# Kernel optimization log

Measured on AMD Instinct MI355X. Metric: run time of the kernel, lower is better.

## Reference

```python
import jax, jax.numpy as jnp
import numpy as np

B, S, DIM = 2, 2048, 2048
H, KVH, HD = 16, 4, 128
G = H // KVH  # GQA groups = 4
THETA = 10000.0


def setup_inputs() -> dict:
    key = jax.random.key(0)
    k0, k1, k2, k3, k4 = jax.random.split(key, 5)
    x = jax.random.normal(k0, (B, S, DIM), jnp.float32)
    # RoPE table: [max_seq_len, head_dim//2, 2] holding (cos, sin)
    inv_freq = 1.0 / (THETA ** (jnp.arange(0, HD, 2, dtype=jnp.float32) / HD))
    angles = jnp.outer(jnp.arange(S, dtype=jnp.float32), inv_freq)  # [S, HD//2]
    freqs_cis = jnp.stack([jnp.cos(angles), jnp.sin(angles)], axis=-1)
    sc = 0.02
    wq = jax.random.normal(k1, (H * HD, DIM), jnp.float32) * sc
    wk = jax.random.normal(k2, (KVH * HD, DIM), jnp.float32) * sc
    wv = jax.random.normal(k3, (KVH * HD, DIM), jnp.float32) * sc
    wo = jax.random.normal(k4, (DIM, H * HD), jnp.float32) * sc
    return {"x": x, "freqs_cis": freqs_cis, "wq": wq, "wk": wk, "wv": wv, "wo": wo}


def apply_rope(x, freqs_cis):
    # x: [B, S, h, HD]; freqs_cis: [max_S, HD//2, 2]
    s = x.shape[1]
    xr = x.astype(jnp.float32).reshape(*x.shape[:-1], -1, 2)  # [B,S,h,HD//2,2]
    cos = freqs_cis[:s, :, 0][None, :, None, :]  # [1,S,1,HD//2]
    sin = freqs_cis[:s, :, 1][None, :, None, :]
    x0, x1 = xr[..., 0], xr[..., 1]
    out = jnp.stack([x0 * cos - x1 * sin, x0 * sin + x1 * cos], axis=-1)
    return out.reshape(x.shape).astype(x.dtype)


def reference(x, freqs_cis, wq, wk, wv, wo):
    b, s, d = x.shape
    q = (x @ wq.T).reshape(b, s, H, HD)
    k = (x @ wk.T).reshape(b, s, KVH, HD)
    v = (x @ wv.T).reshape(b, s, KVH, HD)
    q = apply_rope(q, freqs_cis)
    k = apply_rope(k, freqs_cis)
    # GQA expand: repeat_interleave along head dim
    k = jnp.repeat(k, G, axis=2)  # [b,s,H,HD]
    v = jnp.repeat(v, G, axis=2)
    q = jnp.swapaxes(q, 1, 2)  # [b,H,s,HD]
    k = jnp.swapaxes(k, 1, 2)
    v = jnp.swapaxes(v, 1, 2)
    scale = 1.0 / jnp.sqrt(jnp.asarray(HD, dtype=q.dtype))
    scores = jnp.einsum('bhqd,bhkd->bhqk', q, k) * scale  # [b,H,s,s]
    causal = jnp.tril(jnp.ones((s, s), dtype=bool))
    scores = jnp.where(causal[None, None], scores, jnp.finfo(scores.dtype).min)
    probs = jax.nn.softmax(scores, axis=-1)
    attn = jnp.einsum('bhqk,bhkd->bhqd', probs, v)  # [b,H,s,HD]
    attn = jnp.swapaxes(attn, 1, 2).reshape(b, s, H * HD)
    return attn @ wo.T
```

## Files before the change

### kernel.cpp

```cpp
#include <hip/hip_runtime.h>
#include <stdint.h>

#define B_ 2
#define S_ 2048
#define DIM_ 2048
#define H_ 16
#define KVH_ 4
#define HD_ 128

typedef short short8 __attribute__((ext_vector_type(8)));
typedef float f4 __attribute__((ext_vector_type(4)));
typedef float f16v __attribute__((ext_vector_type(16)));
typedef unsigned int uint2v __attribute__((ext_vector_type(2)));
typedef unsigned short u16;

#define KSCALE (0.08838834764831845f * 1.4426950408889634f)

__device__ __forceinline__ float bf2f(u16 u) {
    union { unsigned int i; float f; } c; c.i = ((unsigned int)u) << 16; return c.f;
}
__device__ __forceinline__ u16 f2bf(float f) {
    union { float f; unsigned int i; } c; c.f = f;
    return (u16)((c.i + 0x7fffu + ((c.i >> 16) & 1u)) >> 16);
}
__device__ __forceinline__ unsigned pk_bf16(float lo, float hi) {
    unsigned r;
    asm("v_cvt_pk_bf16_f32 %0, %1, %2" : "=v"(r) : "v"(lo), "v"(hi));
    return r;
}

#define GLDS16(gp, lp) \
    __builtin_amdgcn_global_load_lds((const __attribute__((address_space(1))) unsigned int*)(gp), \
                                     (__attribute__((address_space(3))) unsigned int*)(lp), 16, 0, 0)

#define BAR()     asm volatile("s_barrier" ::: "memory")
#define WAITLGKM() asm volatile("s_waitcnt lgkmcnt(0)" ::: "memory")
#define SCHEDB()  __builtin_amdgcn_sched_barrier(0)

__global__ void cast_all(const float* __restrict__ x,  const float* __restrict__ wq,
                         const float* __restrict__ wk, const float* __restrict__ wv,
                         const float* __restrict__ wo,
                         u16* __restrict__ xb, u16* __restrict__ wqkvb, u16* __restrict__ wob) {
    int i = blockIdx.x * 256 + threadIdx.x;
    const float4* src; ushort4* dst; int j;
    if (i < 2097152)      { src = (const float4*)x;  dst = (ushort4*)xb;                 j = i; }
    else if (i < 3145728) { src = (const float4*)wq; dst = (ushort4*)wqkvb;              j = i - 2097152; }
    else if (i < 3407872) { src = (const float4*)wk; dst = (ushort4*)wqkvb + 1048576;    j = i - 3145728; }
    else if (i < 3670016) { src = (const float4*)wv; dst = (ushort4*)wqkvb + 1310720;    j = i - 3407872; }
    else                  { src = (const float4*)wo; dst = (ushort4*)wob;                j = i - 3670016; }
    float4 v = src[j];
    ushort4 o;
    o.x = f2bf(v.x); o.y = f2bf(v.y); o.z = f2bf(v.z); o.w = f2bf(v.w);
    dst[j] = o;
}

template<bool OUT_BF16, int NBX>
__global__ __launch_bounds__(512, 2) void gemm256(const u16* __restrict__ A,
                                                  const u16* __restrict__ W,
                                                  void* __restrict__ Cout,
                                                  int M, int N, int K) {
    __shared__ u16 As[2][16384];
    __shared__ u16 Bs[2][16384];
    int t = threadIdx.x, lane = t & 63, w = t >> 6;
    int quad = lane >> 4, l16 = lane & 15, l7 = lane & 7;
    int wm = w >> 2, wn = w & 3;
    int bid = blockIdx.x;
    int xcd = bid & 7, grp = bid >> 3;
    int bx = grp % NBX, by = (grp / NBX) * 8 + xcd;
    size_t m0 = (size_t)by * 256, n0 = (size_t)bx * 256;

    int srow = lane >> 3;
    int sunit = (lane & 7) ^ srow;
    int rR0a = (w >> 2) * 64 + (w & 3) * 8;
    const u16* Ag = A + (m0 + srow) * (size_t)K + sunit * 8;
    const u16* Bg = W + (n0 + srow) * (size_t)K + sunit * 8;

#define STG_A(pl, tk, r0) GLDS16(Ag + ((size_t)((r0) + w * 8)) * K + (tk) * 64, (pl) + ((r0) + w * 8) * 64)
#define STG_B(pl, tk, r0) GLDS16(Bg + ((size_t)((r0) + w * 8)) * K + (tk) * 64, (pl) + ((r0) + w * 8) * 64)
#define STG_BR(pl, tk, bse) GLDS16(Bg + ((size_t)((bse) + rR0a)) * K + (tk) * 64, (pl) + ((bse) + rR0a) * 64)

#define LDA(mh) { \
    _Pragma("unroll") for (int i_ = 0; i_ < 4; i_++) \
    _Pragma("unroll") for (int k_ = 0; k_ < 2; k_++) \
        a[i_][k_] = *(const short8*)&pAc[(wm * 128 + (mh) * 64 + i_ * 16 + l16) * 64 + (((quad + 4 * k_) ^ l7) << 3)]; }
#define LDB(nh) { \
    _Pragma("unroll") for (int j_ = 0; j_ < 2; j_++) \
    _Pragma("unroll") for (int k_ = 0; k_ < 2; k_++) \
        b[j_][k_] = *(const short8*)&pBc[(wn * 64 + (nh) * 32 + j_ * 16 + l16) * 64 + (((quad + 4 * k_) ^ l7) << 3)]; }
#define MFMA_Q(mh, nh) { \
    __builtin_amdgcn_s_setprio(1); \
    _Pragma("unroll") for (int i_ = 0; i_ < 4; i_++) \
    _Pragma("unroll") for (int j_ = 0; j_ < 2; j_++) \
    _Pragma("unroll") for (int k_ = 0; k_ < 2; k_++) \
        acc[(mh) * 4 + i_][(nh) * 2 + j_] = __builtin_amdgcn_mfma_f32_16x16x32_bf16( \
            a[i_][k_], b[j_][k_], acc[(mh) * 4 + i_][(nh) * 2 + j_], 0, 0, 0); \
    __builtin_amdgcn_s_setprio(0); }

    f4 acc[8][4];
    #pragma unroll
    for (int i = 0; i < 8; i++)
        #pragma unroll
        for (int j = 0; j < 4; j++) acc[i][j] = (f4){0.f, 0.f, 0.f, 0.f};

    int NT = K >> 6;

    #pragma unroll
    for (int pt = 0; pt < 2; pt++) {
        u16* pa = &As[pt][0]; u16* pb = &Bs[pt][0];
        #pragma unroll
        for (int r0 = 0; r0 < 256; r0 += 64) { STG_A(pa, pt, r0); STG_B(pb, pt, r0); }
    }
    asm volatile("s_waitcnt vmcnt(0)" ::: "memory");
    BAR();

    short8 a[4][2], b[2][2];
    for (int tt = 0; tt < NT; tt++) {
        int c = tt & 1, nc = c ^ 1;
        u16* pAc = &As[c][0];  u16* pBc = &Bs[c][0];
        u16* pAn = &As[nc][0]; u16* pBn = &Bs[nc][0];
        bool s1 = (tt >= 1) & (tt + 1 < NT);
        bool s2 = (tt + 2 < NT);
        LDA(0); LDB(0);
        if (s1) { STG_A(pAn, tt + 1, 64); STG_A(pAn, tt + 1, 192); }
        BAR(); WAITLGKM(); MFMA_Q(0, 0); BAR();
        LDB(1);
        if (s1) { STG_BR(pBn, tt + 1, 32); STG_BR(pBn, tt + 1, 160); }
        BAR(); WAITLGKM(); MFMA_Q(0, 1); BAR();
        LDA(1); LDB(0);
        if (s2) { STG_A(pAc, tt + 2, 0); STG_A(pAc, tt + 2, 128); }
        BAR(); WAITLGKM(); MFMA_Q(1, 0); BAR();
        if (s2) asm volatile("s_waitcnt vmcnt(2)" ::: "memory");
        else    asm volatile("s_waitcnt vmcnt(0)" ::: "memory");
        LDB(1);
        if (s2) { STG_BR(pBc, tt + 2, 0); STG_BR(pBc, tt + 2, 128); }
        BAR(); WAITLGKM(); MFMA_Q(1, 1); BAR();
    }

    #pragma unroll
    for (int i = 0; i < 8; i++) {
        size_t row = m0 + wm * 128 + i * 16 + quad * 4;
        #pragma unroll
        for (int j = 0; j < 4; j++) {
            size_t col = n0 + wn * 64 + j * 16 + l16;
            #pragma unroll
            for (int r = 0; r < 4; r++) {
                if (OUT_BF16) ((u16*)Cout)[(row + r) * (size_t)N + col] = f2bf(acc[i][j][r]);
                else          ((float*)Cout)[(row + r) * (size_t)N + col] = acc[i][j][r];
            }
        }
    }
#undef STG_A
#undef STG_B
#undef STG_BR
#undef LDA
#undef LDB
#undef MFMA_Q
}

__global__ __launch_bounds__(256) void pack_k(const u16* __restrict__ QKV,
                                              const float* __restrict__ freqs,
                                              u16* __restrict__ Kp) {
    int gid = blockIdx.x * 256 + threadIdx.x;
    int lane = gid & 63, j = (gid >> 6) & 1, ds = (gid >> 7) & 7;
    int kt = (gid >> 10) & 31, bk = gid >> 15;
    int b = bk >> 2, kvh = bk & 3;
    int l31 = lane & 31, hi = lane >> 5;
    int s = kt * 64 + j * 32 + l31;
    int d0 = ds * 16 + hi * 8;
    const u16* src = QKV + (size_t)(b * S_ + s) * 3072 + 2048 + kvh * HD_ + d0;
    short8 v = *(const short8*)src;
    short8 o;
    #pragma unroll
    for (int jp = 0; jp < 4; jp++) {
        float2 cw = ((const float2*)freqs)[s * 64 + ds * 8 + hi * 4 + jp];
        float x0 = bf2f((u16)v[2 * jp]), x1 = bf2f((u16)v[2 * jp + 1]);
        o[2 * jp]     = (short)f2bf(x0 * cw.x - x1 * cw.y);
        o[2 * jp + 1] = (short)f2bf(x0 * cw.y + x1 * cw.x);
    }
    *(short8*)&Kp[(size_t)gid * 8] = o;
}

__global__ __launch_bounds__(256) void pack_v(const u16* __restrict__ QKV, u16* __restrict__ Vp) {
    __shared__ u16 L[64 * 136];
    int bid = blockIdx.x;
    int bk = bid & 7, kt = bid >> 3;
    int b = bk >> 2, kvh = bk & 3;
    int t = threadIdx.x;
    const u16* src = QKV + (size_t)(b * S_ + kt * 64) * 3072 + 2560 + kvh * HD_;
    #pragma unroll
    for (int it = 0; it < 4; it++) {
        int idx = t + it * 256;
        int r = idx >> 4, c = idx & 15;
        *(short8*)&L[r * 136 + c * 8] = *(const short8*)(src + (size_t)r * 3072 + c * 8);
    }
    __syncthreads();
    u16* dst = Vp + (size_t)(bk * 32 + kt) * 8192;
    #pragma unroll
    for (int it = 0; it < 4; it++) {
        int idx = t + it * 256;
        int frag = idx >> 6, lane = idx & 63;
        int ks = frag >> 2, ht = frag & 3;
        int hd = ht * 32 + (lane & 31);
        int k0 = ks * 16 + (lane >> 5) * 8;
        short8 v;
        #pragma unroll
        for (int jj = 0; jj < 8; jj++) v[jj] = (short)L[(k0 + jj) * 136 + hd];
        *(short8*)&dst[(size_t)idx * 8] = v;
    }
}

__global__ __launch_bounds__(64, 1)
void attn_kernel(const u16* __restrict__ QKV,
                 const float* __restrict__ freqs,
                 const u16* __restrict__ Kp,
                 const u16* __restrict__ Vp,
                 u16* __restrict__ Ob) {
    int bid = blockIdx.x;
    int k8 = bid >> 8;
    int c  = bid & 255;
    int bk = c & 7, h4 = (c >> 3) & 3, tq = c >> 5;
    int qb = 63 - (k8 * 8 + ((k8 & 1) ? 7 - tq : tq));
    int b = bk >> 2, kvh = bk & 3;
    int lane = threadIdx.x;
    int l31 = lane & 31, hi = lane >> 5;
    int h = kvh * 4 + h4;
    int nkt = (qb >> 1) + 1;

    short8 qf[8];
    {
        int s = qb * 32 + l31;
        const u16* qp = QKV + ((size_t)(b * S_ + s)) * 3072 + h * HD_ + hi * 8;
        const float2* fr2 = (const float2*)freqs;
        #pragma unroll
        for (int ds = 0; ds < 8; ds++) {
            short8 v = *(const short8*)(qp + ds * 16);
            short8 o;
            #pragma unroll
            for (int jp = 0; jp < 4; jp++) {
                float2 cs = fr2[s * 64 + ds * 8 + hi * 4 + jp];
                float x0 = bf2f((u16)v[2 * jp]), x1 = bf2f((u16)v[2 * jp + 1]);
                o[2 * jp]     = (short)f2bf((x0 * cs.x - x1 * cs.y) * KSCALE);
                o[2 * jp + 1] = (short)f2bf((x0 * cs.y + x1 * cs.x) * KSCALE);
            }
            qf[ds] = o;
        }
    }

    float m_i = -3e38f, ls = 0.f;
    f16v o4[4];
    #pragma unroll
    for (int i = 0; i < 4; i++)
        #pragma unroll
        for (int r = 0; r < 16; r++) o4[i][r] = 0.f;

    const u16* Kpb = Kp + (size_t)bk * 32 * 8192 + lane * 8;
    const u16* Vpb = Vp + (size_t)bk * 32 * 8192 + lane * 8;

    short8 kf[16];
    #pragma unroll
    for (int f = 0; f < 16; f++) kf[f] = *(const short8*)(Kpb + f * 512);

    for (int kt = 0; kt < nkt; kt++) {
        short8 vf[16];
        {
            const u16* vb = Vpb + (size_t)kt * 8192;
            #pragma unroll
            for (int f = 0; f < 16; f++) vf[f] = *(const short8*)(vb + f * 512);
        }
        SCHEDB();

        f16v sA[2], sB[2];
        #pragma unroll
        for (int k2 = 0; k2 < 2; k2++)
            #pragma unroll
            for (int r = 0; r < 16; r++) { sA[k2][r] = 0.f; sB[k2][r] = 0.f; }
        __builtin_amdgcn_s_setprio(1);
        #pragma unroll
        for (int ds = 0; ds < 4; ds++) {
            sA[0] = __builtin_amdgcn_mfma_f32_32x32x16_bf16(kf[ds * 2],     qf[ds], sA[0], 0, 0, 0);
            sA[1] = __builtin_amdgcn_mfma_f32_32x32x16_bf16(kf[ds * 2 + 1], qf[ds], sA[1], 0, 0, 0);
            sB[0] = __builtin_amdgcn_mfma_f32_32x32x16_bf16(kf[(ds + 4) * 2],     qf[ds + 4], sB[0], 0, 0, 0);
            sB[1] = __builtin_amdgcn_mfma_f32_32x32x16_bf16(kf[(ds + 4) * 2 + 1], qf[ds + 4], sB[1], 0, 0, 0);
        }
        __builtin_amdgcn_s_setprio(0);
        SCHEDB();

        if (kt + 1 < nkt) {
            const u16* kb = Kpb + (size_t)(kt + 1) * 8192;
            #pragma unroll
            for (int f = 0; f < 16; f++) kf[f] = *(const short8*)(kb + f * 512);
        }
        SCHEDB();

        f16v sacc[2];
        #pragma unroll
        for (int k2 = 0; k2 < 2; k2++)
            #pragma unroll
            for (int r = 0; r < 16; r++) sacc[k2][r] = sA[k2][r] + sB[k2][r];

        if (kt == nkt - 1) {
            int off0 = kt * 64 - qb * 32;
            #pragma unroll
            for (int k2 = 0; k2 < 2; k2++) {
                #pragma unroll
                for (int r = 0; r < 16; r++) {
                    int colo = off0 + k2 * 32 + (r & 3) + ((r >> 2) << 3) + (hi << 2);
                    if (colo > l31) sacc[k2][r] = -3e38f;
                }
            }
        }

        float mx[16];
        #pragma unroll
        for (int r = 0; r < 16; r++) mx[r] = fmaxf(sacc[0][r], sacc[1][r]);
        #pragma unroll
        for (int s_ = 8; s_ > 0; s_ >>= 1)
            #pragma unroll
            for (int r = 0; r < s_; r++) mx[r] = fmaxf(mx[r], mx[r + s_]);
        float pm = fmaxf(mx[0], __shfl_xor(mx[0], 32, 64));
        if (__any(pm > m_i + 8.0f)) {
            float mnew = fmaxf(m_i, pm);
            float al = exp2f(m_i - mnew);
            ls *= al;
            #pragma unroll
            for (int i = 0; i < 4; i++)
                #pragma unroll
                for (int r = 0; r < 16; r++) o4[i][r] *= al;
            m_i = mnew;
        }

        short8 pa[4];
        #pragma unroll
        for (int k2 = 0; k2 < 2; k2++) {
            float p[16];
            #pragma unroll
            for (int r = 0; r < 16; r++) p[r] = exp2f(sacc[k2][r] - m_i);
            float s0 = (p[0] + p[1]) + (p[2] + p[3]);
            float s1 = (p[4] + p[5]) + (p[6] + p[7]);
            float s2 = (p[8] + p[9]) + (p[10] + p[11]);
            float s3 = (p[12] + p[13]) + (p[14] + p[15]);
            ls += (s0 + s1) + (s2 + s3);
            unsigned W0 = pk_bf16(p[0], p[1]),   W1 = pk_bf16(p[2], p[3]);
            unsigned W2 = pk_bf16(p[4], p[5]),   W3 = pk_bf16(p[6], p[7]);
            unsigned W4 = pk_bf16(p[8], p[9]),   W5 = pk_bf16(p[10], p[11]);
            unsigned W6 = pk_bf16(p[12], p[13]), W7 = pk_bf16(p[14], p[15]);
            uint2v r02 = __builtin_amdgcn_permlane32_swap(W0, W2, false, false);
            uint2v r13 = __builtin_amdgcn_permlane32_swap(W1, W3, false, false);
            uint2v r46 = __builtin_amdgcn_permlane32_swap(W4, W6, false, false);
            uint2v r57 = __builtin_amdgcn_permlane32_swap(W5, W7, false, false);
            union { unsigned u[4]; short8 s8; } flo, fhi;
            flo.u[0] = r02[0]; flo.u[1] = r13[0]; flo.u[2] = r02[1]; flo.u[3] = r13[1];
            fhi.u[0] = r46[0]; fhi.u[1] = r57[0]; fhi.u[2] = r46[1]; fhi.u[3] = r57[1];
            pa[k2 * 2]     = flo.s8;
            pa[k2 * 2 + 1] = fhi.s8;
        }
        SCHEDB();

        __builtin_amdgcn_s_setprio(1);
        #pragma unroll
        for (int ks = 0; ks < 4; ks++) {
            #pragma unroll
            for (int ht = 0; ht < 4; ht++)
                o4[ht] = __builtin_amdgcn_mfma_f32_32x32x16_bf16(vf[ks * 4 + ht], pa[ks], o4[ht], 0, 0, 0);
        }
        __builtin_amdgcn_s_setprio(0);
    }

    ls += __shfl_xor(ls, 32, 64);
    float rl = 1.0f / ls;
    size_t row = (size_t)b * S_ + qb * 32 + l31;
    u16* op = Ob + row * 2048 + h * HD_;
    #pragma unroll
    for (int ht = 0; ht < 4; ht++) {
        #pragma unroll
        for (int g = 0; g < 4; g++) {
            ushort4 st;
            st.x = f2bf(o4[ht][4 * g + 0] * rl);
            st.y = f2bf(o4[ht][4 * g + 1] * rl);
            st.z = f2bf(o4[ht][4 * g + 2] * rl);
            st.w = f2bf(o4[ht][4 * g + 3] * rl);
            *(ushort4*)&op[ht * 32 + g * 8 + hi * 4] = st;
        }
    }
}

extern "C" void kernel_launch(void* const* d_in, const int* in_sizes, int n_in,
                              void* d_out, int out_size, void* d_ws, size_t ws_size,
                              hipStream_t stream) {
    const float* x     = (const float*)d_in[0];
    const float* freqs = (const float*)d_in[1];
    const float* wq    = (const float*)d_in[2];
    const float* wk    = (const float*)d_in[3];
    const float* wv    = (const float*)d_in[4];
    const float* wo    = (const float*)d_in[5];
    float* out = (float*)d_out;

    char* p = (char*)d_ws;
    u16* xb    = (u16*)p; p += (size_t)4096 * 2048 * 2;
    u16* wqkvb = (u16*)p; p += (size_t)3072 * 2048 * 2;
    u16* wob   = (u16*)p; p += (size_t)2048 * 2048 * 2;
    u16* QKVb  = (u16*)p; p += (size_t)4096 * 3072 * 2;
    u16* Kpb   = (u16*)p; p += (size_t)8 * 32 * 8192 * 2;
    u16* Vpb   = (u16*)p; p += (size_t)8 * 32 * 8192 * 2;
    u16* attnb = xb;

    cast_all<<<18432, 256, 0, stream>>>(x, wq, wk, wv, wo, xb, wqkvb, wob);

    gemm256<true, 12><<<192, 512, 0, stream>>>(xb, wqkvb, QKVb, 4096, 3072, 2048);

    pack_k<<<1024, 256, 0, stream>>>(QKVb, freqs, Kpb);
    pack_v<<<256, 256, 0, stream>>>(QKVb, Vpb);

    attn_kernel<<<2048, 64, 0, stream>>>(QKVb, freqs, Kpb, Vpb, attnb);

    gemm256<false, 8><<<128, 512, 0, stream>>>(attnb, wob, out, 4096, 2048, 2048);
}
```

Measured before the change: 318.0 us.

## Split long causal query blocks across two KV chunks with a combine kernel

Query blocks in the upper half of the sequence (qb 32..63) now have their KV loop split into two workgroups, one covering KV tiles 0-15 and one covering the rest. Each writes unnormalized fp32 partial outputs plus its running max and sum to workspace, and a new combine kernel rescales and merges the pairs. The aim is to balance work across the grid and shorten the critical-path workgroups of the causal attention. The cost is an extra kernel launch, partial-output writes and reads, and a path that only runs when the workspace is large enough.

Result: slower. 352.1 us (+10.7%).

```diff
diff --git a/kernel.cpp b/kernel.cpp
--- a/kernel.cpp
+++ b/kernel.cpp
@@ -214,12 +214,34 @@
                  const float* __restrict__ freqs,
                  const u16* __restrict__ Kp,
                  const u16* __restrict__ Vp,
-                 u16* __restrict__ Ob) {
+                 u16* __restrict__ Ob,
+                 float* __restrict__ Po,
+                 float* __restrict__ Pm,
+                 int split) {
     int bid = blockIdx.x;
-    int k8 = bid >> 8;
-    int c  = bid & 255;
-    int bk = c & 7, h4 = (c >> 3) & 3, tq = c >> 5;
-    int qb = 63 - (k8 * 8 + ((k8 & 1) ? 7 - tq : tq));
+    int bk, h4, qb, kt0, kt1, slot = -1;
+    if (split) {
+        int c = bid & 255, t = bid >> 8;
+        bk = c & 7; h4 = (c >> 3) & 3;
+        int tau = t * 8 + (c >> 5);
+        if (tau < 64) {
+            qb = 32 + (tau >> 1);
+            int nkt_ = (qb >> 1) + 1;
+            int ck = tau & 1;
+            kt0 = ck ? 16 : 0;
+            kt1 = ck ? nkt_ : 16;
+            slot = ((bk * 4 + h4) * 32 + (qb - 32)) * 2 + ck;
+        } else {
+            qb = tau - 64;
+            kt0 = 0; kt1 = (qb >> 1) + 1;
+        }
+    } else {
+        int k8 = bid >> 8, c = bid & 255;
+        bk = c & 7; h4 = (c >> 3) & 3;
+        int tq = c >> 5;
+        qb = 63 - (k8 * 8 + ((k8 & 1) ? 7 - tq : tq));
+        kt0 = 0; kt1 = (qb >> 1) + 1;
+    }
     int b = bk >> 2, kvh = bk & 3;
     int lane = threadIdx.x;
     int l31 = lane & 31, hi = lane >> 5;
@@ -257,10 +279,13 @@
     const u16* Vpb = Vp + (size_t)bk * 32 * 8192 + lane * 8;
 
     short8 kf[16];
-    #pragma unroll
-    for (int f = 0; f < 16; f++) kf[f] = *(const short8*)(Kpb + f * 512);
-
-    for (int kt = 0; kt < nkt; kt++) {
+    {
+        const u16* kb = Kpb + (size_t)kt0 * 8192;
+        #pragma unroll
+        for (int f = 0; f < 16; f++) kf[f] = *(const short8*)(kb + f * 512);
+    }
+
+    for (int kt = kt0; kt < kt1; kt++) {
         short8 vf[16];
         {
             const u16* vb = Vpb + (size_t)kt * 8192;
@@ -285,7 +310,7 @@
         __builtin_amdgcn_s_setprio(0);
         SCHEDB();
 
-        if (kt + 1 < nkt) {
+        if (kt + 1 < kt1) {
             const u16* kb = Kpb + (size_t)(kt + 1) * 8192;
             #pragma unroll
             for (int f = 0; f < 16; f++) kf[f] = *(const short8*)(kb + f * 512);
@@ -367,18 +392,63 @@
     }
 
     ls += __shfl_xor(ls, 32, 64);
-    float rl = 1.0f / ls;
+    if (slot >= 0) {
+        float* po = Po + (size_t)slot * 4096 + lane * 64;
+        #pragma unroll
+        for (int ht = 0; ht < 4; ht++)
+            #pragma unroll
+            for (int r = 0; r < 16; r++) po[ht * 16 + r] = o4[ht][r];
+        Pm[(size_t)slot * 128 + lane * 2]     = m_i;
+        Pm[(size_t)slot * 128 + lane * 2 + 1] = ls;
+    } else {
+        float rl = 1.0f / ls;
+        size_t row = (size_t)b * S_ + qb * 32 + l31;
+        u16* op = Ob + row * 2048 + h * HD_;
+        #pragma unroll
+        for (int ht = 0; ht < 4; ht++) {
+            #pragma unroll
+            for (int g = 0; g < 4; g++) {
+                ushort4 st;
+                st.x = f2bf(o4[ht][4 * g + 0] * rl);
+                st.y = f2bf(o4[ht][4 * g + 1] * rl);
+                st.z = f2bf(o4[ht][4 * g + 2] * rl);
+                st.w = f2bf(o4[ht][4 * g + 3] * rl);
+                *(ushort4*)&op[ht * 32 + g * 8 + hi * 4] = st;
+            }
+        }
+    }
+}
+
+__global__ __launch_bounds__(64) void attn_combine(const float* __restrict__ Po,
+                                                   const float* __restrict__ Pm,
+                                                   u16* __restrict__ Ob) {
+    int cid = blockIdx.x;
+    int bk = cid & 7, h4 = (cid >> 3) & 3, qq = cid >> 5;
+    int qb = 32 + qq;
+    int b = bk >> 2, kvh = bk & 3;
+    int h = kvh * 4 + h4;
+    int lane = threadIdx.x;
+    int l31 = lane & 31, hi = lane >> 5;
+    int s0 = ((bk * 4 + h4) * 32 + qq) * 2;
+    float m0 = Pm[(size_t)s0 * 128 + lane * 2],       l0 = Pm[(size_t)s0 * 128 + lane * 2 + 1];
+    float m1 = Pm[(size_t)(s0 + 1) * 128 + lane * 2], l1 = Pm[(size_t)(s0 + 1) * 128 + lane * 2 + 1];
+    float M  = fmaxf(m0, m1);
+    float a0 = exp2f(m0 - M), a1 = exp2f(m1 - M);
+    float rl = 1.0f / (l0 * a0 + l1 * a1);
+    const float4* q0 = (const float4*)(Po + (size_t)s0 * 4096 + lane * 64);
+    const float4* q1 = (const float4*)(Po + (size_t)(s0 + 1) * 4096 + lane * 64);
     size_t row = (size_t)b * S_ + qb * 32 + l31;
     u16* op = Ob + row * 2048 + h * HD_;
     #pragma unroll
     for (int ht = 0; ht < 4; ht++) {
         #pragma unroll
         for (int g = 0; g < 4; g++) {
+            float4 v0 = q0[ht * 4 + g], v1 = q1[ht * 4 + g];
             ushort4 st;
-            st.x = f2bf(o4[ht][4 * g + 0] * rl);
-            st.y = f2bf(o4[ht][4 * g + 1] * rl);
-            st.z = f2bf(o4[ht][4 * g + 2] * rl);
-            st.w = f2bf(o4[ht][4 * g + 3] * rl);
+            st.x = f2bf((v0.x * a0 + v1.x * a1) * rl);
+            st.y = f2bf((v0.y * a0 + v1.y * a1) * rl);
+            st.z = f2bf((v0.z * a0 + v1.z * a1) * rl);
+            st.w = f2bf((v0.w * a0 + v1.w * a1) * rl);
             *(ushort4*)&op[ht * 32 + g * 8 + hi * 4] = st;
         }
     }
@@ -402,7 +472,12 @@
     u16* QKVb  = (u16*)p; p += (size_t)4096 * 3072 * 2;
     u16* Kpb   = (u16*)p; p += (size_t)8 * 32 * 8192 * 2;
     u16* Vpb   = (u16*)p; p += (size_t)8 * 32 * 8192 * 2;
+    float* Po  = (float*)p; p += (size_t)2048 * 4096 * 4;
+    float* Pm  = (float*)p; p += (size_t)2048 * 128 * 4;
     u16* attnb = xb;
+
+    size_t need = (size_t)(p - (char*)d_ws);
+    int split = (ws_size >= need) ? 1 : 0;
 
     cast_all<<<18432, 256, 0, stream>>>(x, wq, wk, wv, wo, xb, wqkvb, wob);
 
@@ -411,7 +486,12 @@
     pack_k<<<1024, 256, 0, stream>>>(QKVb, freqs, Kpb);
     pack_v<<<256, 256, 0, stream>>>(QKVb, Vpb);
 
-    attn_kernel<<<2048, 64, 0, stream>>>(QKVb, freqs, Kpb, Vpb, attnb);
+    if (split) {
+        attn_kernel<<<3072, 64, 0, stream>>>(QKVb, freqs, Kpb, Vpb, attnb, Po, Pm, 1);
+        attn_combine<<<1024, 64, 0, stream>>>(Po, Pm, attnb);
+    } else {
+        attn_kernel<<<2048, 64, 0, stream>>>(QKVb, freqs, Kpb, Vpb, attnb, Po, Pm, 0);
+    }
 
     gemm256<false, 8><<<128, 512, 0, stream>>>(attnb, wob, out, 4096, 2048, 2048);
 }
```

## Process two adjacent query blocks per wave to reuse K/V fragments

Applied to the files above, without the earlier changes.

Each single-wave block now handles an even and an odd 32-row query block that share the same 64-key tiles. Every loaded K and V fragment therefore feeds twice as many MFMAs, and half as many blocks are launched. The work order is remapped into four balanced ranges to even out the causal load. The cost is a doubled accumulator and Q register footprint, which raises register pressure and may cause spills. With fewer blocks there is also less parallelism to hide latency.

Result: slower. 494.8 us (+55.6%).

```diff
diff --git a/kernel.cpp b/kernel.cpp
--- a/kernel.cpp
+++ b/kernel.cpp
@@ -209,6 +209,43 @@
     }
 }
 
+#define SOFTMAX_PACK(sacc, m_i, ls, o4, pa) { \
+    float mx[16]; \
+    _Pragma("unroll") for (int r = 0; r < 16; r++) mx[r] = fmaxf(sacc[0][r], sacc[1][r]); \
+    _Pragma("unroll") for (int s_ = 8; s_ > 0; s_ >>= 1) \
+        _Pragma("unroll") for (int r = 0; r < s_; r++) mx[r] = fmaxf(mx[r], mx[r + s_]); \
+    float pm = fmaxf(mx[0], __shfl_xor(mx[0], 32, 64)); \
+    if (__any(pm > m_i + 8.0f)) { \
+        float mnew = fmaxf(m_i, pm); \
+        float al = exp2f(m_i - mnew); \
+        ls *= al; \
+        _Pragma("unroll") for (int q_ = 0; q_ < 4; q_++) \
+            _Pragma("unroll") for (int r = 0; r < 16; r++) o4[q_][r] *= al; \
+        m_i = mnew; \
+    } \
+    _Pragma("unroll") for (int k2 = 0; k2 < 2; k2++) { \
+        float p[16]; \
+        _Pragma("unroll") for (int r = 0; r < 16; r++) p[r] = exp2f(sacc[k2][r] - m_i); \
+        float s0 = (p[0] + p[1]) + (p[2] + p[3]); \
+        float s1 = (p[4] + p[5]) + (p[6] + p[7]); \
+        float s2 = (p[8] + p[9]) + (p[10] + p[11]); \
+        float s3 = (p[12] + p[13]) + (p[14] + p[15]); \
+        ls += (s0 + s1) + (s2 + s3); \
+        unsigned W0 = pk_bf16(p[0], p[1]),   W1 = pk_bf16(p[2], p[3]); \
+        unsigned W2 = pk_bf16(p[4], p[5]),   W3 = pk_bf16(p[6], p[7]); \
+        unsigned W4 = pk_bf16(p[8], p[9]),   W5 = pk_bf16(p[10], p[11]); \
+        unsigned W6 = pk_bf16(p[12], p[13]), W7 = pk_bf16(p[14], p[15]); \
+        uint2v r02 = __builtin_amdgcn_permlane32_swap(W0, W2, false, false); \
+        uint2v r13 = __builtin_amdgcn_permlane32_swap(W1, W3, false, false); \
+        uint2v r46 = __builtin_amdgcn_permlane32_swap(W4, W6, false, false); \
+        uint2v r57 = __builtin_amdgcn_permlane32_swap(W5, W7, false, false); \
+        union { unsigned u[4]; short8 s8; } flo, fhi; \
+        flo.u[0] = r02[0]; flo.u[1] = r13[0]; flo.u[2] = r02[1]; flo.u[3] = r13[1]; \
+        fhi.u[0] = r46[0]; fhi.u[1] = r57[0]; fhi.u[2] = r46[1]; fhi.u[3] = r57[1]; \
+        pa[k2 * 2]     = flo.s8; \
+        pa[k2 * 2 + 1] = fhi.s8; \
+    } }
+
 __global__ __launch_bounds__(64, 1)
 void attn_kernel(const u16* __restrict__ QKV,
                  const float* __restrict__ freqs,
@@ -216,42 +253,47 @@
                  const u16* __restrict__ Vp,
                  u16* __restrict__ Ob) {
     int bid = blockIdx.x;
-    int k8 = bid >> 8;
-    int c  = bid & 255;
-    int bk = c & 7, h4 = (c >> 3) & 3, tq = c >> 5;
-    int qb = 63 - (k8 * 8 + ((k8 & 1) ? 7 - tq : tq));
+    int c = bid & 255, t = bid >> 8;
+    int bk = c & 7, h4 = (c >> 3) & 3, u = c >> 5;
+    int i = (t == 0) ? (31 - u) : (t == 1) ? (16 + u) : (t == 2) ? (15 - u) : u;
+    int qbE = 2 * i;
+    int nkt = i + 1;
     int b = bk >> 2, kvh = bk & 3;
     int lane = threadIdx.x;
     int l31 = lane & 31, hi = lane >> 5;
     int h = kvh * 4 + h4;
-    int nkt = (qb >> 1) + 1;
-
-    short8 qf[8];
+
+    short8 qE[8], qO[8];
     {
-        int s = qb * 32 + l31;
+        int s = qbE * 32 + l31;
         const u16* qp = QKV + ((size_t)(b * S_ + s)) * 3072 + h * HD_ + hi * 8;
         const float2* fr2 = (const float2*)freqs;
         #pragma unroll
         for (int ds = 0; ds < 8; ds++) {
-            short8 v = *(const short8*)(qp + ds * 16);
-            short8 o;
+            short8 v0 = *(const short8*)(qp + ds * 16);
+            short8 v1 = *(const short8*)(qp + 32 * 3072 + ds * 16);
+            short8 oE, oO;
             #pragma unroll
             for (int jp = 0; jp < 4; jp++) {
-                float2 cs = fr2[s * 64 + ds * 8 + hi * 4 + jp];
-                float x0 = bf2f((u16)v[2 * jp]), x1 = bf2f((u16)v[2 * jp + 1]);
-                o[2 * jp]     = (short)f2bf((x0 * cs.x - x1 * cs.y) * KSCALE);
-                o[2 * jp + 1] = (short)f2bf((x0 * cs.y + x1 * cs.x) * KSCALE);
+                float2 csE = fr2[s * 64 + ds * 8 + hi * 4 + jp];
+                float2 csO = fr2[(s + 32) * 64 + ds * 8 + hi * 4 + jp];
+                float x0 = bf2f((u16)v0[2 * jp]), x1 = bf2f((u16)v0[2 * jp + 1]);
+                oE[2 * jp]     = (short)f2bf((x0 * csE.x - x1 * csE.y) * KSCALE);
+                oE[2 * jp + 1] = (short)f2bf((x0 * csE.y + x1 * csE.x) * KSCALE);
+                float y0 = bf2f((u16)v1[2 * jp]), y1 = bf2f((u16)v1[2 * jp + 1]);
+                oO[2 * jp]     = (short)f2bf((y0 * csO.x - y1 * csO.y) * KSCALE);
+                oO[2 * jp + 1] = (short)f2bf((y0 * csO.y + y1 * csO.x) * KSCALE);
             }
-            qf[ds] = o;
-        }
-    }
-
-    float m_i = -3e38f, ls = 0.f;
-    f16v o4[4];
-    #pragma unroll
-    for (int i = 0; i < 4; i++)
-        #pragma unroll
-        for (int r = 0; r < 16; r++) o4[i][r] = 0.f;
+            qE[ds] = oE; qO[ds] = oO;
+        }
+    }
+
+    float mE = -3e38f, lsE = 0.f, mO = -3e38f, lsO = 0.f;
+    f16v oE4[4], oO4[4];
+    #pragma unroll
+    for (int q_ = 0; q_ < 4; q_++)
+        #pragma unroll
+        for (int r = 0; r < 16; r++) { oE4[q_][r] = 0.f; oO4[q_][r] = 0.f; }
 
     const u16* Kpb = Kp + (size_t)bk * 32 * 8192 + lane * 8;
     const u16* Vpb = Vp + (size_t)bk * 32 * 8192 + lane * 8;
@@ -261,6 +303,22 @@
     for (int f = 0; f < 16; f++) kf[f] = *(const short8*)(Kpb + f * 512);
 
     for (int kt = 0; kt < nkt; kt++) {
+        f16v sE[2], sO[2];
+        #pragma unroll
+        for (int k2 = 0; k2 < 2; k2++)
+            #pragma unroll
+            for (int r = 0; r < 16; r++) { sE[k2][r] = 0.f; sO[k2][r] = 0.f; }
+        __builtin_amdgcn_s_setprio(1);
+        #pragma unroll
+        for (int ds = 0; ds < 8; ds++) {
+            sE[0] = __builtin_amdgcn_mfma_f32_32x32x16_bf16(kf[ds * 2],     qE[ds], sE[0], 0, 0, 0);
+            sE[1] = __builtin_amdgcn_mfma_f32_32x32x16_bf16(kf[ds * 2 + 1], qE[ds], sE[1], 0, 0, 0);
+            sO[0] = __builtin_amdgcn_mfma_f32_32x32x16_bf16(kf[ds * 2],     qO[ds], sO[0], 0, 0, 0);
+            sO[1] = __builtin_amdgcn_mfma_f32_32x32x16_bf16(kf[ds * 2 + 1], qO[ds], sO[1], 0, 0, 0);
+        }
+        __builtin_amdgcn_s_setprio(0);
+        SCHEDB();
+
         short8 vf[16];
         {
             const u16* vb = Vpb + (size_t)kt * 8192;
@@ -269,22 +327,6 @@
         }
         SCHEDB();
 
-        f16v sA[2], sB[2];
-        #pragma unroll
-        for (int k2 = 0; k2 < 2; k2++)
-            #pragma unroll
-            for (int r = 0; r < 16; r++) { sA[k2][r] = 0.f; sB[k2][r] = 0.f; }
-        __builtin_amdgcn_s_setprio(1);
-        #pragma unroll
-        for (int ds = 0; ds < 4; ds++) {
-            sA[0] = __builtin_amdgcn_mfma_f32_32x32x16_bf16(kf[ds * 2],     qf[ds], sA[0], 0, 0, 0);
-            sA[1] = __builtin_amdgcn_mfma_f32_32x32x16_bf16(kf[ds * 2 + 1], qf[ds], sA[1], 0, 0, 0);
-            sB[0] = __builtin_amdgcn_mfma_f32_32x32x16_bf16(kf[(ds + 4) * 2],     qf[ds + 4], sB[0], 0, 0, 0);
-            sB[1] = __builtin_amdgcn_mfma_f32_32x32x16_bf16(kf[(ds + 4) * 2 + 1], qf[ds + 4], sB[1], 0, 0, 0);
-        }
-        __builtin_amdgcn_s_setprio(0);
-        SCHEDB();
-
         if (kt + 1 < nkt) {
             const u16* kb = Kpb + (size_t)(kt + 1) * 8192;
             #pragma unroll
@@ -292,94 +334,53 @@
         }
         SCHEDB();
 
-        f16v sacc[2];
-        #pragma unroll
-        for (int k2 = 0; k2 < 2; k2++)
-            #pragma unroll
-            for (int r = 0; r < 16; r++) sacc[k2][r] = sA[k2][r] + sB[k2][r];
-
         if (kt == nkt - 1) {
-            int off0 = kt * 64 - qb * 32;
-            #pragma unroll
-            for (int k2 = 0; k2 < 2; k2++) {
-                #pragma unroll
-                for (int r = 0; r < 16; r++) {
-                    int colo = off0 + k2 * 32 + (r & 3) + ((r >> 2) << 3) + (hi << 2);
-                    if (colo > l31) sacc[k2][r] = -3e38f;
-                }
+            #pragma unroll
+            for (int r = 0; r < 16; r++) {
+                int colo = (r & 3) + ((r >> 2) << 3) + (hi << 2);
+                if (colo > l31) { sE[0][r] = -3e38f; sO[1][r] = -3e38f; }
+                sE[1][r] = -3e38f;
             }
         }
 
-        float mx[16];
-        #pragma unroll
-        for (int r = 0; r < 16; r++) mx[r] = fmaxf(sacc[0][r], sacc[1][r]);
-        #pragma unroll
-        for (int s_ = 8; s_ > 0; s_ >>= 1)
-            #pragma unroll
-            for (int r = 0; r < s_; r++) mx[r] = fmaxf(mx[r], mx[r + s_]);
-        float pm = fmaxf(mx[0], __shfl_xor(mx[0], 32, 64));
-        if (__any(pm > m_i + 8.0f)) {
-            float mnew = fmaxf(m_i, pm);
-            float al = exp2f(m_i - mnew);
-            ls *= al;
-            #pragma unroll
-            for (int i = 0; i < 4; i++)
-                #pragma unroll
-                for (int r = 0; r < 16; r++) o4[i][r] *= al;
-            m_i = mnew;
-        }
-
-        short8 pa[4];
-        #pragma unroll
-        for (int k2 = 0; k2 < 2; k2++) {
-            float p[16];
-            #pragma unroll
-            for (int r = 0; r < 16; r++) p[r] = exp2f(sacc[k2][r] - m_i);
-            float s0 = (p[0] + p[1]) + (p[2] + p[3]);
-            float s1 = (p[4] + p[5]) + (p[6] + p[7]);
-            float s2 = (p[8] + p[9]) + (p[10] + p[11]);
-            float s3 = (p[12] + p[13]) + (p[14] + p[15]);
-            ls += (s0 + s1) + (s2 + s3);
-            unsigned W0 = pk_bf16(p[0], p[1]),   W1 = pk_bf16(p[2], p[3]);
-            unsigned W2 = pk_bf16(p[4], p[5]),   W3 = pk_bf16(p[6], p[7]);
-            unsigned W4 = pk_bf16(p[8], p[9]),   W5 = pk_bf16(p[10], p[11]);
-            unsigned W6 = pk_bf16(p[12], p[13]), W7 = pk_bf16(p[14], p[15]);
-            uint2v r02 = __builtin_amdgcn_permlane32_swap(W0, W2, false, false);
-            uint2v r13 = __builtin_amdgcn_permlane32_swap(W1, W3, false, false);
-            uint2v r46 = __builtin_amdgcn_permlane32_swap(W4, W6, false, false);
-            uint2v r57 = __builtin_amdgcn_permlane32_swap(W5, W7, false, false);
-            union { unsigned u[4]; short8 s8; } flo, fhi;
-            flo.u[0] = r02[0]; flo.u[1] = r13[0]; flo.u[2] = r02[1]; flo.u[3] = r13[1];
-            fhi.u[0] = r46[0]; fhi.u[1] = r57[0]; fhi.u[2] = r46[1]; fhi.u[3] = r57[1];
-            pa[k2 * 2]     = flo.s8;
-            pa[k2 * 2 + 1] = fhi.s8;
-        }
+        short8 paE[4], paO[4];
+        SOFTMAX_PACK(sE, mE, lsE, oE4, paE);
+        SOFTMAX_PACK(sO, mO, lsO, oO4, paO);
         SCHEDB();
 
         __builtin_amdgcn_s_setprio(1);
         #pragma unroll
         for (int ks = 0; ks < 4; ks++) {
             #pragma unroll
-            for (int ht = 0; ht < 4; ht++)
-                o4[ht] = __builtin_amdgcn_mfma_f32_32x32x16_bf16(vf[ks * 4 + ht], pa[ks], o4[ht], 0, 0, 0);
+            for (int ht = 0; ht < 4; ht++) {
+                oE4[ht] = __builtin_amdgcn_mfma_f32_32x32x16_bf16(vf[ks * 4 + ht], paE[ks], oE4[ht], 0, 0, 0);
+                oO4[ht] = __builtin_amdgcn_mfma_f32_32x32x16_bf16(vf[ks * 4 + ht], paO[ks], oO4[ht], 0, 0, 0);
+            }
         }
         __builtin_amdgcn_s_setprio(0);
     }
 
-    ls += __shfl_xor(ls, 32, 64);
-    float rl = 1.0f / ls;
-    size_t row = (size_t)b * S_ + qb * 32 + l31;
-    u16* op = Ob + row * 2048 + h * HD_;
+    lsE += __shfl_xor(lsE, 32, 64);
+    lsO += __shfl_xor(lsO, 32, 64);
+    float rlE = 1.0f / lsE, rlO = 1.0f / lsO;
+    size_t row = (size_t)b * S_ + qbE * 32 + l31;
+    u16* opE = Ob + row * 2048 + h * HD_;
+    u16* opO = opE + (size_t)32 * 2048;
     #pragma unroll
     for (int ht = 0; ht < 4; ht++) {
         #pragma unroll
         for (int g = 0; g < 4; g++) {
-            ushort4 st;
-            st.x = f2bf(o4[ht][4 * g + 0] * rl);
-            st.y = f2bf(o4[ht][4 * g + 1] * rl);
-            st.z = f2bf(o4[ht][4 * g + 2] * rl);
-            st.w = f2bf(o4[ht][4 * g + 3] * rl);
-            *(ushort4*)&op[ht * 32 + g * 8 + hi * 4] = st;
+            ushort4 stE, stO;
+            stE.x = f2bf(oE4[ht][4 * g + 0] * rlE);
+            stE.y = f2bf(oE4[ht][4 * g + 1] * rlE);
+            stE.z = f2bf(oE4[ht][4 * g + 2] * rlE);
+            stE.w = f2bf(oE4[ht][4 * g + 3] * rlE);
+            *(ushort4*)&opE[ht * 32 + g * 8 + hi * 4] = stE;
+            stO.x = f2bf(oO4[ht][4 * g + 0] * rlO);
+            stO.y = f2bf(oO4[ht][4 * g + 1] * rlO);
+            stO.z = f2bf(oO4[ht][4 * g + 2] * rlO);
+            stO.w = f2bf(oO4[ht][4 * g + 3] * rlO);
+            *(ushort4*)&opO[ht * 32 + g * 8 + hi * 4] = stO;
         }
     }
 }
@@ -411,7 +412,7 @@
     pack_k<<<1024, 256, 0, stream>>>(QKVb, freqs, Kpb);
     pack_v<<<256, 256, 0, stream>>>(QKVb, Vpb);
 
-    attn_kernel<<<2048, 64, 0, stream>>>(QKVb, freqs, Kpb, Vpb, attnb);
+    attn_kernel<<<1024, 64, 0, stream>>>(QKVb, freqs, Kpb, Vpb, attnb);
 
     gemm256<false, 8><<<128, 512, 0, stream>>>(attnb, wob, out, 4096, 2048, 2048);
 }
```
